# Optimization experiments

Hardware: AMD Instinct MI355X
Metric: run time of the kernel (lower is better)

The kernel has to match this reference:

```python
import jax, jax.numpy as jnp
import numpy as np

SCALING = 32.0 / 16.0  # alpha / rank

def setup_inputs() -> dict:
    key = jax.random.key(0)
    ks = jax.random.split(key, 6)
    B, S, D_IN, D_OUT, R, N_ADAPT = 32, 1024, 1024, 4096, 16, 8
    hidden_states = jax.random.normal(ks[0], (B, S, D_IN), dtype=jnp.float32)
    adapter_ids = jax.random.randint(ks[1], (B,), 0, N_ADAPT, dtype=jnp.int32)
    W = jax.random.normal(ks[2], (D_IN, D_OUT), dtype=jnp.float32) * 0.02
    bias = jax.random.normal(ks[3], (D_OUT,), dtype=jnp.float32) * 0.02
    lora_a = jax.random.normal(ks[4], (N_ADAPT, D_IN, R), dtype=jnp.float32) * (1.0 / np.sqrt(D_IN))
    lora_b = jax.random.normal(ks[5], (N_ADAPT, R, D_OUT), dtype=jnp.float32) * 0.02
    return {"hidden_states": hidden_states, "adapter_ids": adapter_ids,
            "W": W, "bias": bias, "lora_a": lora_a, "lora_b": lora_b}

def reference(hidden_states, adapter_ids, W, bias, lora_a, lora_b):
    # Base GPT-2 Conv1D: x @ W + b, W: [in, out]
    base_out = jnp.einsum('bsd,do->bso', hidden_states, W) + bias
    # Per-sample routed LoRA: gather each sample's adapter A/B, then batched low-rank matmuls.
    # Equivalent to the torch loop over unique adapter ids with mask/scatter (dropout=0, eval).
    a_sel = lora_a[adapter_ids]  # [B, d_in, r]
    b_sel = lora_b[adapter_ids]  # [B, r, d_out]
    low_rank = jnp.einsum('bsd,bdr->bsr', hidden_states, a_sel)
    delta = jnp.einsum('bsr,bro->bso', low_rank, b_sel) * SCALING
    return base_out + delta
```

## Files before the change

kernel.cpp:

```cpp
#include <hip/hip_runtime.h>
#include <hip/hip_bf16.h>
#include <stdint.h>

constexpr int kB = 32;
constexpr int kS = 1024;
constexpr int kDin = 1024;
constexpr int kDout = 4096;
constexpr int kRank = 16;
constexpr int kNAdapt = 8;
constexpr int kM = kB * kS;
constexpr float kScale = 2.0f;

typedef __attribute__((ext_vector_type(4))) float f32x4;
typedef __attribute__((ext_vector_type(8))) short s16x8;
typedef __attribute__((ext_vector_type(8))) unsigned short u16x8;
typedef __attribute__((ext_vector_type(4))) unsigned short u16x4;

__device__ __forceinline__ unsigned short f2bf(float f) {
  union { float f; uint32_t u; } x; x.f = f;
  uint32_t u = x.u;
  u += 0x7fffu + ((u >> 16) & 1u);
  return (unsigned short)(u >> 16);
}

constexpr int kWeffBlocks = kNAdapt * (kDin / 64) * (kDout / 64);
constexpr int kCastBlocks = 2048;

__global__ __launch_bounds__(256) void prep_kernel(
    const float* __restrict__ h, unsigned short* __restrict__ hout,
    const float* __restrict__ W, const float* __restrict__ la,
    const float* __restrict__ lb, unsigned short* __restrict__ weff) {
  __shared__ float Wt[64][68];
  __shared__ float At[64][20];
  __shared__ float Bt[16][68];
  int bid = blockIdx.x;
  int t = threadIdx.x;
  if (bid >= kWeffBlocks) {
    int cb = bid - kWeffBlocks;
    size_t base = (size_t)cb * 256 + t;
    constexpr size_t stride = (size_t)kCastBlocks * 256;
    constexpr size_t total8 = (size_t)kM * kDin / 8;
#pragma unroll
    for (int p = 0; p < 8; ++p) {
      size_t i = base + p * stride;
      if (i < total8) {
        const f32x4* src = reinterpret_cast<const f32x4*>(h) + i * 2;
        f32x4 v0 = src[0], v1 = src[1];
        u16x8 r;
        r[0] = f2bf(v0[0]); r[1] = f2bf(v0[1]); r[2] = f2bf(v0[2]); r[3] = f2bf(v0[3]);
        r[4] = f2bf(v1[0]); r[5] = f2bf(v1[1]); r[6] = f2bf(v1[2]); r[7] = f2bf(v1[3]);
        *reinterpret_cast<u16x8*>(hout + i * 8) = r;
      }
    }
    return;
  }
  int e = bid & 7;
  int rem = bid >> 3;
  int dt = rem >> 6;
  int ot = rem & 63;
  int d0 = dt * 64, o0 = ot * 64;
  {
    int r = t >> 4;
    int c = (t & 15) * 4;
    const float* wp = W + (size_t)(d0 + r) * kDout + o0 + c;
#pragma unroll
    for (int p = 0; p < 4; ++p) {
      f32x4 v = *reinterpret_cast<const f32x4*>(wp + (size_t)p * 16 * kDout);
      *reinterpret_cast<f32x4*>(&Wt[p * 16 + r][c]) = v;
    }
  }
  {
    int d = t >> 2, r4 = (t & 3) * 4;
    f32x4 v = *reinterpret_cast<const f32x4*>(la + ((size_t)e * kDin + d0 + d) * kRank + r4);
    *reinterpret_cast<f32x4*>(&At[d][r4]) = v;
  }
  {
    int r = t >> 4, c = (t & 15) * 4;
    f32x4 v = *reinterpret_cast<const f32x4*>(lb + ((size_t)e * kRank + r) * kDout + o0 + c);
    *reinterpret_cast<f32x4*>(&Bt[r][c]) = v;
  }
  __syncthreads();
  int ol_base = t >> 4;
  int dl = (t & 15) * 4;
  f32x4 areg[4][4];
#pragma unroll
  for (int j = 0; j < 4; ++j)
#pragma unroll
    for (int q = 0; q < 4; ++q)
      areg[j][q] = *reinterpret_cast<const f32x4*>(&At[dl + j][q * 4]);
#pragma unroll
  for (int p = 0; p < 4; ++p) {
    int ol = p * 16 + ol_base;
    float bv[kRank];
#pragma unroll
    for (int r = 0; r < kRank; ++r) bv[r] = Bt[r][ol];
    u16x4 r4;
#pragma unroll
    for (int j = 0; j < 4; ++j) {
      float acc = 0.f;
#pragma unroll
      for (int q = 0; q < 4; ++q)
        acc += areg[j][q][0] * bv[q * 4 + 0] + areg[j][q][1] * bv[q * 4 + 1] +
               areg[j][q][2] * bv[q * 4 + 2] + areg[j][q][3] * bv[q * 4 + 3];
      r4[j] = f2bf(Wt[dl + j][ol] + kScale * acc);
    }
    *reinterpret_cast<u16x4*>(weff + ((size_t)e * kDout + o0 + ol) * kDin + d0 + dl) = r4;
  }
}

constexpr int BM = 256, BN = 256, BK = 64;
constexpr int MT2 = kM / BM;
constexpr int NT2 = kDout / BN;
constexpr int NWG2 = MT2 * NT2;

__device__ __forceinline__ void gload16(const unsigned short* g, unsigned short* l) {
  __builtin_amdgcn_global_load_lds((const __attribute__((address_space(1))) void*)g,
                                   (__attribute__((address_space(3))) void*)l, 16, 0, 0);
}

#define STG_A(s, kk) do { \
  gload16(gA + (size_t)0 * kDin + (kk) * 64, ldst + (s) * 16384); \
  gload16(gA + (size_t)64 * kDin + (kk) * 64, ldst + (s) * 16384 + 4096); \
  gload16(gA + (size_t)128 * kDin + (kk) * 64, ldst + (s) * 16384 + 8192); \
  gload16(gA + (size_t)192 * kDin + (kk) * 64, ldst + (s) * 16384 + 12288); \
} while (0)
#define STG_B(s, kk) do { \
  gload16(gB + (size_t)0 * kDin + (kk) * 64, ldst + 49152 + (s) * 16384); \
  gload16(gB + (size_t)64 * kDin + (kk) * 64, ldst + 49152 + (s) * 16384 + 4096); \
  gload16(gB + (size_t)128 * kDin + (kk) * 64, ldst + 49152 + (s) * 16384 + 8192); \
  gload16(gB + (size_t)192 * kDin + (kk) * 64, ldst + 49152 + (s) * 16384 + 12288); \
} while (0)

#define RD_A(mh, s) do { _Pragma("unroll") for (int ii = 0; ii < 4; ++ii) { \
  a[ii][0] = *(const s16x8*)&lds[(s) * 16384 + aRow + ((mh) * 4 + ii) * 1024 + e0]; \
  a[ii][1] = *(const s16x8*)&lds[(s) * 16384 + aRow + ((mh) * 4 + ii) * 1024 + e1]; } } while (0)
#define RD_B(nh, breg, s) do { _Pragma("unroll") for (int jj = 0; jj < 2; ++jj) { \
  breg[jj][0] = *(const s16x8*)&lds[49152 + (s) * 16384 + bRow + ((nh) * 2 + jj) * 1024 + e0]; \
  breg[jj][1] = *(const s16x8*)&lds[49152 + (s) * 16384 + bRow + ((nh) * 2 + jj) * 1024 + e1]; } } while (0)

#define MMQ(mh, nh, breg) do { \
  _Pragma("unroll") for (int ii = 0; ii < 4; ++ii) \
  _Pragma("unroll") for (int jj = 0; jj < 2; ++jj) { \
    acc[(mh) * 4 + ii][(nh) * 2 + jj] = __builtin_amdgcn_mfma_f32_16x16x32_bf16( \
        a[ii][0], breg[jj][0], acc[(mh) * 4 + ii][(nh) * 2 + jj], 0, 0, 0); \
    acc[(mh) * 4 + ii][(nh) * 2 + jj] = __builtin_amdgcn_mfma_f32_16x16x32_bf16( \
        a[ii][1], breg[jj][1], acc[(mh) * 4 + ii][(nh) * 2 + jj], 0, 0, 0); } \
} while (0)

#define VMC(n) asm volatile("s_waitcnt vmcnt(" #n ")" ::: "memory")

__global__ __launch_bounds__(512, 2) void gemm256_kernel(
    const unsigned short* __restrict__ Ab,
    const unsigned short* __restrict__ Weff,
    const float* __restrict__ bias,
    const int* __restrict__ aids,
    float* __restrict__ out) {
  __shared__ unsigned short lds[81920];
  int bid = blockIdx.x;
  int swz = (bid & 7) * (NWG2 / 8) + (bid >> 3);
  int mt = swz >> 4, nt = swz & 15;
  int aid = aids[mt >> 2];
  const unsigned short* Aptr = Ab + (size_t)mt * BM * kDin;
  const unsigned short* Bptr = Weff + ((size_t)aid * kDout + (size_t)nt * BN) * kDin;

  int t = threadIdx.x;
  int l = t & 63;
  int w = t >> 6;
  int wm = w >> 2;
  int wn = w & 3;

  int srcColEl = ((t & 7) * 8) ^ (((t >> 3) & 7) << 3);
  const unsigned short* gA = Aptr + (size_t)(t >> 3) * kDin + srcColEl;
  const unsigned short* gB = Bptr + (size_t)(t >> 3) * kDin + srcColEl;
  unsigned short* ldst = lds + t * 8;

  int xmEl = (l & 7) << 3;
  int e0 = (((l >> 4) * 8) ^ xmEl);
  int e1 = e0 ^ 32;
  int aRow = (wm * 128 + (l & 15)) * 64;
  int bRow = (wn * 64 + (l & 15)) * 64;

  f32x4 acc[8][4];
#pragma unroll
  for (int m = 0; m < 8; ++m)
#pragma unroll
    for (int n = 0; n < 4; ++n) acc[m][n] = f32x4{0.f, 0.f, 0.f, 0.f};
  s16x8 a[4][2], b0[2][2], b1[2][2];

  STG_A(0, 0); STG_B(0, 0); STG_A(1, 1);

#pragma unroll
  for (int kt = 0; kt < 16; ++kt) {
    const int sa = kt % 3;
    const int sb = kt & 1;
    if (kt < 15) { VMC(4); } else { VMC(0); }
    __builtin_amdgcn_s_barrier();
    __builtin_amdgcn_sched_barrier(0);
    if (kt < 15) STG_B((kt + 1) & 1, kt + 1);
    RD_A(0, sa);
    RD_B(0, b0, sb); RD_B(1, b1, sb);
    MMQ(0, 0, b0); MMQ(0, 1, b1);
    RD_A(1, sa);
    MMQ(1, 0, b0); MMQ(1, 1, b1);
    if (kt < 14) STG_A((kt + 2) % 3, kt + 2);
  }

  size_t row0 = (size_t)mt * BM + wm * 128 + (l >> 4) * 4;
  int col0 = nt * BN + wn * 64 + (l & 15);
#pragma unroll
  for (int nf = 0; nf < 4; ++nf) {
    float bv = bias[col0 + nf * 16];
#pragma unroll
    for (int mf = 0; mf < 8; ++mf) {
#pragma unroll
      for (int j = 0; j < 4; ++j)
        out[(row0 + mf * 16 + j) * kDout + col0 + nf * 16] = acc[mf][nf][j] + bv;
    }
  }
}

extern "C" void kernel_launch(void* const* d_in, const int* in_sizes, int n_in,
                              void* d_out, int out_size, void* d_ws, size_t ws_size,
                              hipStream_t stream) {
  const float* h    = (const float*)d_in[0];
  const int*   aids = (const int*)d_in[1];
  const float* W    = (const float*)d_in[2];
  const float* bias = (const float*)d_in[3];
  const float* la   = (const float*)d_in[4];
  const float* lb   = (const float*)d_in[5];
  float* out = (float*)d_out;

  unsigned short* Abf  = (unsigned short*)d_ws;
  unsigned short* Weff = Abf + (size_t)kM * kDin;

  prep_kernel<<<kWeffBlocks + kCastBlocks, 256, 0, stream>>>(h, Abf, W, la, lb, Weff);
  gemm256_kernel<<<NWG2, 512, 0, stream>>>(Abf, Weff, bias, aids, out);
}
```

Baseline: 427.7 us.

## Split GEMM tile across 16 waves with smaller per-wave subtiles and setprio

Doubles the GEMM workgroup to 1024 threads so each of 16 waves computes a 64x64 sub-tile instead of 128x64, halving accumulator and A-fragment registers and halving per-thread global-to-LDS loads. It also raises wave priority around the MFMA block. The aim is more latency hiding and less register pressure, at the cost of lower per-wave register reuse, more total LDS reads per tile, and heavier barriers.

```diff
diff --git a/kernel.cpp b/kernel.cpp
--- a/kernel.cpp
+++ b/kernel.cpp
@@ -119,37 +119,33 @@
 }
 
 #define STG_A(s, kk) do { \
-  gload16(gA + (size_t)0 * kDin + (kk) * 64, ldst + (s) * 16384); \
-  gload16(gA + (size_t)64 * kDin + (kk) * 64, ldst + (s) * 16384 + 4096); \
+  gload16(gA + (kk) * 64, ldst + (s) * 16384); \
   gload16(gA + (size_t)128 * kDin + (kk) * 64, ldst + (s) * 16384 + 8192); \
-  gload16(gA + (size_t)192 * kDin + (kk) * 64, ldst + (s) * 16384 + 12288); \
 } while (0)
 #define STG_B(s, kk) do { \
-  gload16(gB + (size_t)0 * kDin + (kk) * 64, ldst + 49152 + (s) * 16384); \
-  gload16(gB + (size_t)64 * kDin + (kk) * 64, ldst + 49152 + (s) * 16384 + 4096); \
+  gload16(gB + (kk) * 64, ldst + 49152 + (s) * 16384); \
   gload16(gB + (size_t)128 * kDin + (kk) * 64, ldst + 49152 + (s) * 16384 + 8192); \
-  gload16(gB + (size_t)192 * kDin + (kk) * 64, ldst + 49152 + (s) * 16384 + 12288); \
 } while (0)
 
-#define RD_A(mh, s) do { _Pragma("unroll") for (int ii = 0; ii < 4; ++ii) { \
-  a[ii][0] = *(const s16x8*)&lds[(s) * 16384 + aRow + ((mh) * 4 + ii) * 1024 + e0]; \
-  a[ii][1] = *(const s16x8*)&lds[(s) * 16384 + aRow + ((mh) * 4 + ii) * 1024 + e1]; } } while (0)
-#define RD_B(nh, breg, s) do { _Pragma("unroll") for (int jj = 0; jj < 2; ++jj) { \
+#define RD_A2(ah, s) do { _Pragma("unroll") for (int ii = 0; ii < 2; ++ii) { \
+  a[ii][0] = *(const s16x8*)&lds[(s) * 16384 + aRow + ((ah) * 2 + ii) * 1024 + e0]; \
+  a[ii][1] = *(const s16x8*)&lds[(s) * 16384 + aRow + ((ah) * 2 + ii) * 1024 + e1]; } } while (0)
+#define RD_B2(nh, breg, s) do { _Pragma("unroll") for (int jj = 0; jj < 2; ++jj) { \
   breg[jj][0] = *(const s16x8*)&lds[49152 + (s) * 16384 + bRow + ((nh) * 2 + jj) * 1024 + e0]; \
   breg[jj][1] = *(const s16x8*)&lds[49152 + (s) * 16384 + bRow + ((nh) * 2 + jj) * 1024 + e1]; } } while (0)
 
-#define MMQ(mh, nh, breg) do { \
-  _Pragma("unroll") for (int ii = 0; ii < 4; ++ii) \
+#define MMQ2(ah, nh, breg) do { \
+  _Pragma("unroll") for (int ii = 0; ii < 2; ++ii) \
   _Pragma("unroll") for (int jj = 0; jj < 2; ++jj) { \
-    acc[(mh) * 4 + ii][(nh) * 2 + jj] = __builtin_amdgcn_mfma_f32_16x16x32_bf16( \
-        a[ii][0], breg[jj][0], acc[(mh) * 4 + ii][(nh) * 2 + jj], 0, 0, 0); \
-    acc[(mh) * 4 + ii][(nh) * 2 + jj] = __builtin_amdgcn_mfma_f32_16x16x32_bf16( \
-        a[ii][1], breg[jj][1], acc[(mh) * 4 + ii][(nh) * 2 + jj], 0, 0, 0); } \
+    acc[(ah) * 2 + ii][(nh) * 2 + jj] = __builtin_amdgcn_mfma_f32_16x16x32_bf16( \
+        a[ii][0], breg[jj][0], acc[(ah) * 2 + ii][(nh) * 2 + jj], 0, 0, 0); \
+    acc[(ah) * 2 + ii][(nh) * 2 + jj] = __builtin_amdgcn_mfma_f32_16x16x32_bf16( \
+        a[ii][1], breg[jj][1], acc[(ah) * 2 + ii][(nh) * 2 + jj], 0, 0, 0); } \
 } while (0)
 
 #define VMC(n) asm volatile("s_waitcnt vmcnt(" #n ")" ::: "memory")
 
-__global__ __launch_bounds__(512, 2) void gemm256_kernel(
+__global__ __launch_bounds__(1024, 4) void gemm256_kernel(
     const unsigned short* __restrict__ Ab,
     const unsigned short* __restrict__ Weff,
     const float* __restrict__ bias,
@@ -177,15 +173,15 @@
   int xmEl = (l & 7) << 3;
   int e0 = (((l >> 4) * 8) ^ xmEl);
   int e1 = e0 ^ 32;
-  int aRow = (wm * 128 + (l & 15)) * 64;
+  int aRow = (wm * 64 + (l & 15)) * 64;
   int bRow = (wn * 64 + (l & 15)) * 64;
 
-  f32x4 acc[8][4];
-#pragma unroll
-  for (int m = 0; m < 8; ++m)
+  f32x4 acc[4][4];
+#pragma unroll
+  for (int m = 0; m < 4; ++m)
 #pragma unroll
     for (int n = 0; n < 4; ++n) acc[m][n] = f32x4{0.f, 0.f, 0.f, 0.f};
-  s16x8 a[4][2], b0[2][2], b1[2][2];
+  s16x8 a[2][2], b0[2][2], b1[2][2];
 
   STG_A(0, 0); STG_B(0, 0); STG_A(1, 1);
 
@@ -193,25 +189,27 @@
   for (int kt = 0; kt < 16; ++kt) {
     const int sa = kt % 3;
     const int sb = kt & 1;
-    if (kt < 15) { VMC(4); } else { VMC(0); }
+    if (kt < 15) { VMC(2); } else { VMC(0); }
     __builtin_amdgcn_s_barrier();
     __builtin_amdgcn_sched_barrier(0);
     if (kt < 15) STG_B((kt + 1) & 1, kt + 1);
-    RD_A(0, sa);
-    RD_B(0, b0, sb); RD_B(1, b1, sb);
-    MMQ(0, 0, b0); MMQ(0, 1, b1);
-    RD_A(1, sa);
-    MMQ(1, 0, b0); MMQ(1, 1, b1);
+    RD_A2(0, sa);
+    RD_B2(0, b0, sb); RD_B2(1, b1, sb);
+    __builtin_amdgcn_s_setprio(1);
+    MMQ2(0, 0, b0); MMQ2(0, 1, b1);
+    RD_A2(1, sa);
+    MMQ2(1, 0, b0); MMQ2(1, 1, b1);
+    __builtin_amdgcn_s_setprio(0);
     if (kt < 14) STG_A((kt + 2) % 3, kt + 2);
   }
 
-  size_t row0 = (size_t)mt * BM + wm * 128 + (l >> 4) * 4;
+  size_t row0 = (size_t)mt * BM + wm * 64 + (l >> 4) * 4;
   int col0 = nt * BN + wn * 64 + (l & 15);
 #pragma unroll
   for (int nf = 0; nf < 4; ++nf) {
     float bv = bias[col0 + nf * 16];
 #pragma unroll
-    for (int mf = 0; mf < 8; ++mf) {
+    for (int mf = 0; mf < 4; ++mf) {
 #pragma unroll
       for (int j = 0; j < 4; ++j)
         out[(row0 + mf * 16 + j) * kDout + col0 + nf * 16] = acc[mf][nf][j] + bv;
@@ -234,5 +232,5 @@
   unsigned short* Weff = Abf + (size_t)kM * kDin;
 
   prep_kernel<<<kWeffBlocks + kCastBlocks, 256, 0, stream>>>(h, Abf, W, la, lb, Weff);
-  gemm256_kernel<<<NWG2, 512, 0, stream>>>(Abf, Weff, bias, aids, out);
-}
+  gemm256_kernel<<<NWG2, 1024, 0, stream>>>(Abf, Weff, bias, aids, out);
+}
```

Result: slower. 654.6 us (+53.1%).

## Replace per-adapter merged weights with shared base GEMM plus low-rank MFMA epilogue

Applied to the files above, without the earlier changes.

Instead of building eight merged bf16 weight matrices W+scale*A·B (one per adapter), the prep kernel now transposes W to bf16 once, precomputes the rank-16 projection h·A per row (padded to 32), and packs scaled B per adapter. The GEMM reads only the shared W and adds the LoRA delta as one extra K=32 MFMA step in the epilogue. This shrinks the weight working set so B tiles are reused across all batches in L2, and cuts prep work. In exchange, prep has to read h a second time for the low-rank projection, and that projection is rounded to bf16.

```diff
diff --git a/kernel.cpp b/kernel.cpp
--- a/kernel.cpp
+++ b/kernel.cpp
@@ -22,21 +22,75 @@
   u += 0x7fffu + ((u >> 16) & 1u);
   return (unsigned short)(u >> 16);
 }
-
-constexpr int kWeffBlocks = kNAdapt * (kDin / 64) * (kDout / 64);
+__device__ __forceinline__ float bf2f(unsigned short b) {
+  union { uint32_t u; float f; } x; x.u = (uint32_t)b << 16; return x.f;
+}
+
+constexpr int kWtBlocks = (kDin / 64) * (kDout / 64);
+constexpr int kLbpBlocks = kNAdapt * kDout / 256;
 constexpr int kCastBlocks = 2048;
+constexpr int kLrBlocks = kM / 64;
+constexpr int kLbpBase = kWtBlocks;
+constexpr int kCastBase = kLbpBase + kLbpBlocks;
+constexpr int kLrBase = kCastBase + kCastBlocks;
+constexpr int kPrepBlocks = kLrBase + kLrBlocks;
 
 __global__ __launch_bounds__(256) void prep_kernel(
     const float* __restrict__ h, unsigned short* __restrict__ hout,
     const float* __restrict__ W, const float* __restrict__ la,
-    const float* __restrict__ lb, unsigned short* __restrict__ weff) {
+    const float* __restrict__ lb, const int* __restrict__ aids,
+    unsigned short* __restrict__ wt,
+    unsigned short* __restrict__ lrp,
+    unsigned short* __restrict__ lbp) {
   __shared__ float Wt[64][68];
-  __shared__ float At[64][20];
-  __shared__ float Bt[16][68];
+  __shared__ unsigned short laS[16384];
+  __shared__ float redS[4096];
   int bid = blockIdx.x;
   int t = threadIdx.x;
-  if (bid >= kWeffBlocks) {
-    int cb = bid - kWeffBlocks;
+
+  if (bid < kWtBlocks) {
+    int dt = bid >> 6, ot = bid & 63;
+    int d0 = dt * 64, o0 = ot * 64;
+    int r = t >> 4;
+    int c = (t & 15) * 4;
+    const float* wp = W + (size_t)(d0 + r) * kDout + o0 + c;
+#pragma unroll
+    for (int p = 0; p < 4; ++p) {
+      f32x4 v = *reinterpret_cast<const f32x4*>(wp + (size_t)p * 16 * kDout);
+      *reinterpret_cast<f32x4*>(&Wt[p * 16 + r][c]) = v;
+    }
+    __syncthreads();
+    int ol_base = t >> 4;
+    int dl = (t & 15) * 4;
+#pragma unroll
+    for (int p = 0; p < 4; ++p) {
+      int ol = p * 16 + ol_base;
+      u16x4 r4;
+#pragma unroll
+      for (int j = 0; j < 4; ++j) r4[j] = f2bf(Wt[dl + j][ol]);
+      *reinterpret_cast<u16x4*>(wt + (size_t)(o0 + ol) * kDin + d0 + dl) = r4;
+    }
+    return;
+  }
+  if (bid < kCastBase) {
+    int oidx = (bid - kLbpBase) * 256 + t;
+    int e = oidx >> 12, o = oidx & (kDout - 1);
+    u16x8 lo, hi, z;
+#pragma unroll
+    for (int r = 0; r < 8; ++r) {
+      lo[r] = f2bf(kScale * lb[((size_t)e * kRank + r) * kDout + o]);
+      hi[r] = f2bf(kScale * lb[((size_t)e * kRank + 8 + r) * kDout + o]);
+      z[r] = 0;
+    }
+    unsigned short* dst = lbp + (size_t)oidx * 32;
+    *reinterpret_cast<u16x8*>(dst) = lo;
+    *reinterpret_cast<u16x8*>(dst + 8) = hi;
+    *reinterpret_cast<u16x8*>(dst + 16) = z;
+    *reinterpret_cast<u16x8*>(dst + 24) = z;
+    return;
+  }
+  if (bid < kLrBase) {
+    int cb = bid - kCastBase;
     size_t base = (size_t)cb * 256 + t;
     constexpr size_t stride = (size_t)kCastBlocks * 256;
     constexpr size_t total8 = (size_t)kM * kDin / 8;
@@ -46,65 +100,67 @@
       if (i < total8) {
         const f32x4* src = reinterpret_cast<const f32x4*>(h) + i * 2;
         f32x4 v0 = src[0], v1 = src[1];
-        u16x8 r;
-        r[0] = f2bf(v0[0]); r[1] = f2bf(v0[1]); r[2] = f2bf(v0[2]); r[3] = f2bf(v0[3]);
-        r[4] = f2bf(v1[0]); r[5] = f2bf(v1[1]); r[6] = f2bf(v1[2]); r[7] = f2bf(v1[3]);
-        *reinterpret_cast<u16x8*>(hout + i * 8) = r;
+        u16x8 rr;
+        rr[0] = f2bf(v0[0]); rr[1] = f2bf(v0[1]); rr[2] = f2bf(v0[2]); rr[3] = f2bf(v0[3]);
+        rr[4] = f2bf(v1[0]); rr[5] = f2bf(v1[1]); rr[6] = f2bf(v1[2]); rr[7] = f2bf(v1[3]);
+        *reinterpret_cast<u16x8*>(hout + i * 8) = rr;
       }
     }
     return;
   }
-  int e = bid & 7;
-  int rem = bid >> 3;
-  int dt = rem >> 6;
-  int ot = rem & 63;
-  int d0 = dt * 64, o0 = ot * 64;
   {
-    int r = t >> 4;
-    int c = (t & 15) * 4;
-    const float* wp = W + (size_t)(d0 + r) * kDout + o0 + c;
-#pragma unroll
-    for (int p = 0; p < 4; ++p) {
-      f32x4 v = *reinterpret_cast<const f32x4*>(wp + (size_t)p * 16 * kDout);
-      *reinterpret_cast<f32x4*>(&Wt[p * 16 + r][c]) = v;
-    }
-  }
-  {
-    int d = t >> 2, r4 = (t & 3) * 4;
-    f32x4 v = *reinterpret_cast<const f32x4*>(la + ((size_t)e * kDin + d0 + d) * kRank + r4);
-    *reinterpret_cast<f32x4*>(&At[d][r4]) = v;
-  }
-  {
-    int r = t >> 4, c = (t & 15) * 4;
-    f32x4 v = *reinterpret_cast<const f32x4*>(lb + ((size_t)e * kRank + r) * kDout + o0 + c);
-    *reinterpret_cast<f32x4*>(&Bt[r][c]) = v;
-  }
-  __syncthreads();
-  int ol_base = t >> 4;
-  int dl = (t & 15) * 4;
-  f32x4 areg[4][4];
-#pragma unroll
-  for (int j = 0; j < 4; ++j)
-#pragma unroll
-    for (int q = 0; q < 4; ++q)
-      areg[j][q] = *reinterpret_cast<const f32x4*>(&At[dl + j][q * 4]);
-#pragma unroll
-  for (int p = 0; p < 4; ++p) {
-    int ol = p * 16 + ol_base;
-    float bv[kRank];
-#pragma unroll
-    for (int r = 0; r < kRank; ++r) bv[r] = Bt[r][ol];
-    u16x4 r4;
-#pragma unroll
-    for (int j = 0; j < 4; ++j) {
-      float acc = 0.f;
-#pragma unroll
-      for (int q = 0; q < 4; ++q)
-        acc += areg[j][q][0] * bv[q * 4 + 0] + areg[j][q][1] * bv[q * 4 + 1] +
-               areg[j][q][2] * bv[q * 4 + 2] + areg[j][q][3] * bv[q * 4 + 3];
-      r4[j] = f2bf(Wt[dl + j][ol] + kScale * acc);
-    }
-    *reinterpret_cast<u16x4*>(weff + ((size_t)e * kDout + o0 + ol) * kDin + d0 + dl) = r4;
+    int j = bid - kLrBase;
+    int row0 = j * 64;
+    int e = aids[row0 >> 10];
+    const float* lap = la + (size_t)e * kDin * kRank;
+#pragma unroll
+    for (int c = 0; c < 16; ++c) {
+      f32x4 v = *reinterpret_cast<const f32x4*>(lap + c * 1024 + t * 4);
+      int o = c * 1024 + t * 4;
+      laS[o] = f2bf(v[0]); laS[o + 1] = f2bf(v[1]);
+      laS[o + 2] = f2bf(v[2]); laS[o + 3] = f2bf(v[3]);
+    }
+    __syncthreads();
+    int rq = t >> 2;
+    int q = t & 3;
+    const float* hp0 = h + (size_t)(row0 + rq) * kDin + q * 256;
+    float p[16];
+#pragma unroll
+    for (int r = 0; r < 16; ++r) p[r] = 0.f;
+#pragma unroll
+    for (int c = 0; c < 4; ++c) {
+      f32x4 hv[16];
+#pragma unroll
+      for (int i = 0; i < 16; ++i)
+        hv[i] = *reinterpret_cast<const f32x4*>(hp0 + c * 64 + i * 4);
+#pragma unroll
+      for (int dd = 0; dd < 64; ++dd) {
+        float v = hv[dd >> 2][dd & 3];
+        int d = q * 256 + c * 64 + dd;
+        u16x8 l0 = *reinterpret_cast<const u16x8*>(&laS[d * 16]);
+        u16x8 l1 = *reinterpret_cast<const u16x8*>(&laS[d * 16 + 8]);
+#pragma unroll
+        for (int r = 0; r < 8; ++r) {
+          p[r] += v * bf2f(l0[r]);
+          p[8 + r] += v * bf2f(l1[r]);
+        }
+      }
+    }
+#pragma unroll
+    for (int r = 0; r < 16; ++r) redS[(rq * 4 + q) * 16 + r] = p[r];
+    __syncthreads();
+    int row = t >> 2, rg = (t & 3) * 4;
+    u16x4 outv, zv;
+#pragma unroll
+    for (int k = 0; k < 4; ++k) {
+      float s = redS[(row * 4 + 0) * 16 + rg + k] + redS[(row * 4 + 1) * 16 + rg + k] +
+                redS[(row * 4 + 2) * 16 + rg + k] + redS[(row * 4 + 3) * 16 + rg + k];
+      outv[k] = f2bf(s);
+      zv[k] = 0;
+    }
+    unsigned short* dst = lrp + (size_t)(row0 + row) * 32;
+    *reinterpret_cast<u16x4*>(dst + rg) = outv;
+    *reinterpret_cast<u16x4*>(dst + 16 + rg) = zv;
   }
 }
 
@@ -119,13 +175,13 @@
 }
 
 #define STG_A(s, kk) do { \
-  gload16(gA + (size_t)0 * kDin + (kk) * 64, ldst + (s) * 16384); \
+  gload16(gA + (kk) * 64, ldst + (s) * 16384); \
   gload16(gA + (size_t)64 * kDin + (kk) * 64, ldst + (s) * 16384 + 4096); \
   gload16(gA + (size_t)128 * kDin + (kk) * 64, ldst + (s) * 16384 + 8192); \
   gload16(gA + (size_t)192 * kDin + (kk) * 64, ldst + (s) * 16384 + 12288); \
 } while (0)
 #define STG_B(s, kk) do { \
-  gload16(gB + (size_t)0 * kDin + (kk) * 64, ldst + 49152 + (s) * 16384); \
+  gload16(gB + (kk) * 64, ldst + 49152 + (s) * 16384); \
   gload16(gB + (size_t)64 * kDin + (kk) * 64, ldst + 49152 + (s) * 16384 + 4096); \
   gload16(gB + (size_t)128 * kDin + (kk) * 64, ldst + 49152 + (s) * 16384 + 8192); \
   gload16(gB + (size_t)192 * kDin + (kk) * 64, ldst + 49152 + (s) * 16384 + 12288); \
@@ -151,7 +207,9 @@
 
 __global__ __launch_bounds__(512, 2) void gemm256_kernel(
     const unsigned short* __restrict__ Ab,
-    const unsigned short* __restrict__ Weff,
+    const unsigned short* __restrict__ Wt,
+    const unsigned short* __restrict__ lrp,
+    const unsigned short* __restrict__ lbp,
     const float* __restrict__ bias,
     const int* __restrict__ aids,
     float* __restrict__ out) {
@@ -161,7 +219,7 @@
   int mt = swz >> 4, nt = swz & 15;
   int aid = aids[mt >> 2];
   const unsigned short* Aptr = Ab + (size_t)mt * BM * kDin;
-  const unsigned short* Bptr = Weff + ((size_t)aid * kDout + (size_t)nt * BN) * kDin;
+  const unsigned short* Bptr = Wt + (size_t)nt * BN * kDin;
 
   int t = threadIdx.x;
   int l = t & 63;
@@ -205,6 +263,33 @@
     if (kt < 14) STG_A((kt + 2) % 3, kt + 2);
   }
 
+  __builtin_amdgcn_s_barrier();
+  {
+    const unsigned short* glr = lrp + (size_t)mt * BM * 32;
+    const unsigned short* glb = lbp + ((size_t)aid * kDout + (size_t)nt * BN) * 32;
+    gload16(glr + t * 8, lds + t * 8);
+    gload16(glr + 4096 + t * 8, lds + 4096 + t * 8);
+    gload16(glb + t * 8, lds + 8192 + t * 8);
+    gload16(glb + 4096 + t * 8, lds + 12288 + t * 8);
+  }
+  VMC(0);
+  __builtin_amdgcn_s_barrier();
+  {
+    int kq = (l >> 4) * 8;
+#pragma unroll
+    for (int mf = 0; mf < 8; ++mf)
+      a[mf >> 1][mf & 1] = *(const s16x8*)&lds[(wm * 128 + mf * 16 + (l & 15)) * 32 + kq];
+#pragma unroll
+    for (int nf = 0; nf < 4; ++nf)
+      b0[nf >> 1][nf & 1] = *(const s16x8*)&lds[8192 + (wn * 64 + nf * 16 + (l & 15)) * 32 + kq];
+#pragma unroll
+    for (int mf = 0; mf < 8; ++mf)
+#pragma unroll
+      for (int nf = 0; nf < 4; ++nf)
+        acc[mf][nf] = __builtin_amdgcn_mfma_f32_16x16x32_bf16(
+            a[mf >> 1][mf & 1], b0[nf >> 1][nf & 1], acc[mf][nf], 0, 0, 0);
+  }
+
   size_t row0 = (size_t)mt * BM + wm * 128 + (l >> 4) * 4;
   int col0 = nt * BN + wn * 64 + (l & 15);
 #pragma unroll
@@ -230,9 +315,11 @@
   const float* lb   = (const float*)d_in[5];
   float* out = (float*)d_out;
 
-  unsigned short* Abf  = (unsigned short*)d_ws;
-  unsigned short* Weff = Abf + (size_t)kM * kDin;
-
-  prep_kernel<<<kWeffBlocks + kCastBlocks, 256, 0, stream>>>(h, Abf, W, la, lb, Weff);
-  gemm256_kernel<<<NWG2, 512, 0, stream>>>(Abf, Weff, bias, aids, out);
-}
+  unsigned short* Abf = (unsigned short*)d_ws;
+  unsigned short* WtB = Abf + (size_t)kM * kDin;
+  unsigned short* lrp = WtB + (size_t)kDout * kDin;
+  unsigned short* lbp = lrp + (size_t)kM * 32;
+
+  prep_kernel<<<kPrepBlocks, 256, 0, stream>>>(h, Abf, W, la, lb, aids, WtB, lrp, lbp);
+  gemm256_kernel<<<NWG2, 512, 0, stream>>>(Abf, WtB, lrp, lbp, bias, aids, out);
+}
```

New measurement: 502.0 us. +17.4%, slower.
